# Performance work log

Hardware: AMD Instinct MI355X
Metric: run time of the kernel (lower is better)

## Reference

```python
import jax, jax.numpy as jnp
import numpy as np
from math import sqrt


def _build_transitions(dim):
    # Upper-triangular (i<=j) pairs in the same row-major order as the torch loop.
    iu0, iu1 = np.triu_indices(dim)
    n_mono = len(iu0)
    idx = np.arange(n_mono)
    M = np.zeros((dim, dim), dtype=np.int32)
    M[iu0, iu1] = idx
    M[iu1, iu0] = idx
    coef_trans = np.full((n_mono, 1), sqrt(2.0), dtype=np.float32)
    coef_trans[idx[iu0 == iu1]] = 1.0  # diagonal coefficients stay scale 1
    return iu0, iu1, M.reshape(-1), coef_trans


def setup_inputs() -> dict:
    key = jax.random.key(0)
    k1, k2, k3, k4 = jax.random.split(key, 4)
    dim, n_quadrics, B = 512, 64, 2048
    n_mono = dim * (dim - 1) // 2 + dim  # 131328
    points = jax.random.normal(k1, (B, dim), dtype=jnp.float32)
    # orthogonal-ish init is only an init detail; random normal keeps math identical
    q_coefs = jax.random.normal(k2, (n_mono, n_quadrics), dtype=jnp.float32) / np.sqrt(n_mono)
    l_coefs = 2.0 * jax.random.uniform(k3, (dim, n_quadrics), dtype=jnp.float32) - 1.0
    free_coefs = 2.0 * jax.random.uniform(k4, (1, n_quadrics), dtype=jnp.float32) - 1.0
    return {"points": points, "q_coefs": q_coefs, "l_coefs": l_coefs, "free_coefs": free_coefs}


def reference(points, q_coefs, l_coefs, free_coefs):
    B, dim = points.shape
    nq = q_coefs.shape[1]
    iu0, iu1, inds_trans, coef_trans_np = _build_transitions(dim)
    coef_trans = jnp.asarray(coef_trans_np)

    # quadratic monomials: q[b, k] = p[b, i_k] * p[b, j_k]  (upper-tri order)
    q = points[:, iu0] * points[:, iu1]  # (B, n_mono)

    coefs = q_coefs * coef_trans  # (n_mono, nq) real coefficients

    # values of quadrics at points
    values = jnp.abs(q @ coefs + points @ l_coefs + free_coefs)  # (B, nq)

    # symmetric full matrices gathered from flat coefficient vector
    m_full = coefs[inds_trans].reshape(dim, dim, nq)  # (dim, dim, nq)
    dm = (jnp.eye(dim, dtype=points.dtype) + 1.0)[:, :, None]  # 2 on diag, ... wait: eye+ones -> 2 diag, 1 off
    m_scaled = m_full * dm

    # gradients: grad[b, k, e] = sum_d p[b, d] * m_scaled[d, e, k] + l_coefs[e, k]
    q_grad = jnp.einsum("bd,dek->bke", points, m_scaled) + l_coefs.T[None, :, :]  # (B, nq, dim)
    grad = jnp.sum(q_grad * q_grad, axis=2)  # (B, nq)

    norm = jnp.linalg.norm(q_coefs, axis=0)  # (nq,)
    scores = (jnp.sqrt(grad / 4.0 + values * norm) - jnp.sqrt(grad) / 2.0) / norm
    return scores
```

## Files before the change

kernel.cpp:

```cpp
#include <hip/hip_runtime.h>

#define DIM 512
#define NQ 64
#define BATCH 2048

typedef __bf16  bf16x8  __attribute__((ext_vector_type(8)));
typedef float   floatx4 __attribute__((ext_vector_type(4)));

static __device__ inline unsigned short f2bf(float f) {
    unsigned int u = __float_as_uint(f);
    return (unsigned short)((u + 0x7fffu + ((u >> 16) & 1u)) >> 16);
}
static __device__ inline float bf2f(unsigned short h) {
    return __uint_as_float((unsigned int)h << 16);
}
static __device__ inline unsigned int pack2(float a, float b) {
    return (unsigned)f2bf(a) | ((unsigned)f2bf(b) << 16);
}

__global__ __launch_bounds__(512, 3)
void hsq_expand_kernel(const float* __restrict__ qc,
                       const float* __restrict__ pts,
                       unsigned short* __restrict__ W,
                       unsigned short* __restrict__ Pb,
                       float* __restrict__ npart) {
    const int e = blockIdx.x;

    if (blockIdx.y == 4) {
        const int i4 = e * 512 + threadIdx.x;
        const float4 v = *(const float4*)(pts + (size_t)i4 * 4);
        uint2 wv;
        wv.x = pack2(v.x, v.y); wv.y = pack2(v.z, v.w);
        *(uint2*)(Pb + (size_t)i4 * 4) = wv;
        return;
    }

    const int dblk = blockIdx.y;
    const int pb   = dblk * 512 + e;
    const int tid  = threadIdx.x;
    const int w    = tid >> 6;
    const int lane = tid & 63;
    const int g    = lane >> 4;
    const int u    = lane & 15;
    const int d0   = dblk * 128;

    __shared__ unsigned short tv[64 * 136];
    __shared__ float part2[8][64];

    float4 nacc4 = {0.f, 0.f, 0.f, 0.f};

#pragma unroll
    for (int p = 0; p < 4; ++p) {
        const int rloc = p * 32 + w * 4;
        const int d = d0 + rloc + g;
        const int i = d < e ? d : e;
        const int j = d < e ? e : d;
        const int idx = i * DIM - ((i * (i - 1)) >> 1) + (j - i);
        float4 f = *(const float4*)(qc + (size_t)idx * NQ + u * 4);

        if (d >= e) {
            nacc4.x += f.x * f.x; nacc4.y += f.y * f.y;
            nacc4.z += f.z * f.z; nacc4.w += f.w * f.w;
        }
        const float s = (d == e) ? 2.0f : 1.41421356237309515f;
        float4 v = {f.x * s, f.y * s, f.z * s, f.w * s};

        {
            float s0 = (g & 2) ? v.x : v.z;
            float s1 = (g & 2) ? v.y : v.w;
            const float r0 = __shfl_xor(s0, 32);
            const float r1 = __shfl_xor(s1, 32);
            if (g & 2) { v.x = r0; v.y = r1; } else { v.z = r0; v.w = r1; }
        }
        {
            float s0 = (g & 1) ? v.x : v.y;
            float s1 = (g & 1) ? v.z : v.w;
            const float r0 = __shfl_xor(s0, 16);
            const float r1 = __shfl_xor(s1, 16);
            if (g & 1) { v.x = r0; v.z = r1; } else { v.y = r0; v.w = r1; }
        }
        const int k = u * 4 + g;
        uint2 wv;
        wv.x = pack2(v.x, v.y);
        wv.y = pack2(v.z, v.w);
        *(uint2*)&tv[k * 136 + rloc] = wv;
    }

    nacc4.x += __shfl_xor(nacc4.x, 16); nacc4.y += __shfl_xor(nacc4.y, 16);
    nacc4.z += __shfl_xor(nacc4.z, 16); nacc4.w += __shfl_xor(nacc4.w, 16);
    nacc4.x += __shfl_xor(nacc4.x, 32); nacc4.y += __shfl_xor(nacc4.y, 32);
    nacc4.z += __shfl_xor(nacc4.z, 32); nacc4.w += __shfl_xor(nacc4.w, 32);
    if (g == 0) *(float4*)&part2[w][u * 4] = nacc4;
    __syncthreads();

#pragma unroll
    for (int r = 0; r < 2; ++r) {
        const int kk = r * 32 + (tid >> 4);
        const int uu = tid & 15;
        const uint4 ww = *(const uint4*)&tv[kk * 136 + uu * 8];
        *(uint4*)(W + ((size_t)(kk * DIM + e)) * DIM + dblk * 128 + uu * 8) = ww;
    }
    if (tid < 64) {
        npart[(size_t)tid * 2048 + pb] =
            part2[0][tid] + part2[1][tid] + part2[2][tid] + part2[3][tid] +
            part2[4][tid] + part2[5][tid] + part2[6][tid] + part2[7][tid];
    }
}

__global__ __launch_bounds__(512, 2)
void hsq_gemm_kernel(const unsigned short* __restrict__ Pb,
                     const unsigned short* __restrict__ W,
                     const float* __restrict__ l_coefs,
                     float2* __restrict__ part) {
    extern __shared__ unsigned short smem[];

    const int bid = blockIdx.x;
    const int wg  = (bid & 7) * 128 + (bid >> 3);
    const int k   = wg >> 4;
    const int rem = wg & 15;
    const int et  = rem >> 3;
    const int mt  = rem & 7;
    const int m0  = mt * 256;

    const int tid  = threadIdx.x;
    const int lane = tid & 63;
    const int w    = tid >> 6;
    const int wm   = w >> 2;
    const int wn   = w & 3;
    const int c    = lane & 15;
    const int quad = lane >> 4;

    const unsigned short* Wk = W + ((size_t)k * DIM + (size_t)et * 256) * DIM;

    const int scolb = ((tid & 7) * 16) ^ (((tid >> 3) & 7) << 4);
    const unsigned short* pAs = Pb + (size_t)(m0 + (tid >> 3)) * DIM + (scolb >> 1);
    const unsigned short* pBs = Wk + (size_t)(tid >> 3) * DIM + (scolb >> 1);

    const int xorv  = (c & 7) << 4;
    const int koff0 = ((0 * 64 + quad * 16) ^ xorv) >> 1;
    const int koff1 = ((1 * 64 + quad * 16) ^ xorv) >> 1;
    const int awoff = wm * 8192 + c * 64;
    const int bwoff = (wn >> 1) * 8192 + (wn & 1) * 4096 + c * 64;

#define STAGE_HALF(LDSELEM, GSRC) do {                                         \
    _Pragma("unroll")                                                          \
    for (int cc_ = 0; cc_ < 2; ++cc_) {                                        \
        __builtin_amdgcn_global_load_lds(                                      \
            (const __attribute__((address_space(1))) unsigned int*)            \
                ((GSRC) + (size_t)(cc_ * 64) * DIM),                           \
            (__attribute__((address_space(3))) unsigned int*)                  \
                (smem + (LDSELEM) + cc_ * 4096 + tid * 8),                     \
            16, 0, 0);                                                         \
    }                                                                          \
} while (0)

#define LOADB(BBASE) do {                                                      \
    _Pragma("unroll")                                                          \
    for (int ni_ = 0; ni_ < 4; ++ni_) {                                        \
        bfr[ni_][0] = *(const bf16x8*)(smem + (BBASE) + bwoff + ni_ * 1024 + koff0); \
        bfr[ni_][1] = *(const bf16x8*)(smem + (BBASE) + bwoff + ni_ * 1024 + koff1); \
    }                                                                          \
} while (0)

#define PHASE(ABASE, MI0, PRE_B, STAGE_AND_WAIT) do {                          \
    bf16x8 a00 = *(const bf16x8*)(smem + (ABASE) + awoff + (MI0) * 1024 + koff0);     \
    bf16x8 a01 = *(const bf16x8*)(smem + (ABASE) + awoff + (MI0) * 1024 + koff1);     \
    bf16x8 a10 = *(const bf16x8*)(smem + (ABASE) + awoff + ((MI0) + 1) * 1024 + koff0); \
    bf16x8 a11 = *(const bf16x8*)(smem + (ABASE) + awoff + ((MI0) + 1) * 1024 + koff1); \
    PRE_B;                                                                     \
    STAGE_AND_WAIT;                                                            \
    asm volatile("" ::: "memory");                                             \
    __builtin_amdgcn_s_barrier();                                              \
    asm volatile("" ::: "memory");                                             \
    __builtin_amdgcn_s_setprio(1);                                             \
    _Pragma("unroll")                                                          \
    for (int ni_ = 0; ni_ < 4; ++ni_) {                                        \
        acc[(MI0)][ni_]     = __builtin_amdgcn_mfma_f32_16x16x32_bf16(a00, bfr[ni_][0], acc[(MI0)][ni_], 0, 0, 0);     \
        acc[(MI0)][ni_]     = __builtin_amdgcn_mfma_f32_16x16x32_bf16(a01, bfr[ni_][1], acc[(MI0)][ni_], 0, 0, 0);     \
        acc[(MI0) + 1][ni_] = __builtin_amdgcn_mfma_f32_16x16x32_bf16(a10, bfr[ni_][0], acc[(MI0) + 1][ni_], 0, 0, 0); \
        acc[(MI0) + 1][ni_] = __builtin_amdgcn_mfma_f32_16x16x32_bf16(a11, bfr[ni_][1], acc[(MI0) + 1][ni_], 0, 0, 0); \
    }                                                                          \
    __builtin_amdgcn_s_setprio(0);                                             \
    asm volatile("" ::: "memory");                                             \
    __builtin_amdgcn_s_barrier();                                              \
    asm volatile("" ::: "memory");                                             \
} while (0)

    floatx4 acc[8][4];
#pragma unroll
    for (int mi = 0; mi < 8; ++mi)
#pragma unroll
        for (int ni = 0; ni < 4; ++ni)
            acc[mi][ni] = (floatx4){0.f, 0.f, 0.f, 0.f};

    bf16x8 bfr[4][2];

    STAGE_HALF(0,             pAs);
    STAGE_HALF(8192,          pAs + 128 * DIM);
    STAGE_HALF(16384,         pBs);
    STAGE_HALF(16384 + 8192,  pBs + 128 * DIM);
    STAGE_HALF(49152,         pBs + 64);
    STAGE_HALF(49152 + 8192,  pBs + 128 * DIM + 64);
    asm volatile("s_waitcnt vmcnt(4)" ::: "memory");
    __builtin_amdgcn_s_barrier();
    asm volatile("" ::: "memory");

    for (int it = 0; it < 4; ++it) {
        const unsigned short* pA1 = pAs + (size_t)(2 * it + 1) * 64;
        const unsigned short* pB2 = pBs + (size_t)(2 * it + 2) * 64;
        const unsigned short* pA2 = pAs + (size_t)(2 * it + 2) * 64;
        const unsigned short* pB3 = pBs + (size_t)(2 * it + 3) * 64;

        PHASE(0, 0, LOADB(16384), { STAGE_HALF(32768, pA1); });
        PHASE(0, 2, ((void)0),    { STAGE_HALF(32768 + 8192, pA1 + 128 * DIM); });
        PHASE(0, 4, ((void)0),    { if (it < 3) STAGE_HALF(16384, pB2); });
        PHASE(0, 6, ((void)0), {
            if (it < 3) {
                STAGE_HALF(16384 + 8192, pB2 + 128 * DIM);
                asm volatile("s_waitcnt vmcnt(4)" ::: "memory");
            } else {
                asm volatile("s_waitcnt vmcnt(0)" ::: "memory");
            }
        });
        PHASE(32768, 0, LOADB(49152), { if (it < 3) STAGE_HALF(0, pA2); });
        PHASE(32768, 2, ((void)0),    { if (it < 3) STAGE_HALF(8192, pA2 + 128 * DIM); });
        PHASE(32768, 4, ((void)0),    { if (it < 3) STAGE_HALF(49152, pB3); });
        PHASE(32768, 6, ((void)0), {
            if (it < 3) {
                STAGE_HALF(49152 + 8192, pB3 + 128 * DIM);
                asm volatile("s_waitcnt vmcnt(4)" ::: "memory");
            }
        });
    }
#undef PHASE
#undef LOADB
#undef STAGE_HALF

    __syncthreads();

    float lcv[4];
#pragma unroll
    for (int ni = 0; ni < 4; ++ni)
        lcv[ni] = l_coefs[(et * 256 + wn * 64 + ni * 16 + c) * NQ + k];

    const unsigned short* Pe = Pb + (size_t)(m0 + wm * 128) * DIM + et * 256 + wn * 64 + c;
    float* red = (float*)smem;

#pragma unroll
    for (int mi = 0; mi < 8; ++mi)
#pragma unroll
        for (int r = 0; r < 4; ++r) {
            const unsigned short* Prow = Pe + (size_t)(mi * 16 + quad * 4 + r) * DIM;
            float pv = 0.f, pg = 0.f;
#pragma unroll
            for (int ni = 0; ni < 4; ++ni) {
                const float g = acc[mi][ni][r];
                const float l = lcv[ni];
                pv += bf2f(Prow[ni * 16]) * (0.5f * g + l);
                const float gq = g + l;
                pg += gq * gq;
            }
#pragma unroll
            for (int off = 1; off < 16; off <<= 1) {
                pv += __shfl_xor(pv, off);
                pg += __shfl_xor(pg, off);
            }
            if (c == 0) {
                const int row16 = mi * 16 + quad * 4 + r;
                red[(w * 128 + row16) * 2 + 0] = pv;
                red[(w * 128 + row16) * 2 + 1] = pg;
            }
        }
    __syncthreads();

    if (tid < 256) {
        const int row16 = tid & 127;
        const int wmf   = tid >> 7;
        float pv = 0.f, pg = 0.f;
#pragma unroll
        for (int wnf = 0; wnf < 4; ++wnf) {
            const int wi = wmf * 4 + wnf;
            pv += red[(wi * 128 + row16) * 2 + 0];
            pg += red[(wi * 128 + row16) * 2 + 1];
        }
        part[((size_t)(et * NQ + k)) * BATCH + m0 + wmf * 128 + row16] =
            make_float2(pv, pg);
    }
}

__global__ void hsq_final_kernel(const float2* __restrict__ part,
                                 const float* __restrict__ npart,
                                 const float* __restrict__ free_coefs,
                                 float* __restrict__ out) {
    const int k = blockIdx.x;
    const int t = threadIdx.x;
    __shared__ float ws[4];

    const float4* src = (const float4*)(npart + (size_t)k * 2048);
    const float4 a = src[t * 2], b = src[t * 2 + 1];
    float s = a.x + a.y + a.z + a.w + b.x + b.y + b.z + b.w;
#pragma unroll
    for (int off = 1; off < 64; off <<= 1) s += __shfl_xor(s, off);
    if ((t & 63) == 0) ws[t >> 6] = s;
    __syncthreads();
    const float nrm = sqrtf(ws[0] + ws[1] + ws[2] + ws[3]);
    const float fc  = free_coefs[k];

#pragma unroll
    for (int i = 0; i < 8; ++i) {
        const int bidx = i * 256 + t;
        float pv = 0.f, pg = 0.f;
#pragma unroll
        for (int eb = 0; eb < 2; ++eb) {
            const float2 p = part[((size_t)(eb * NQ + k)) * BATCH + bidx];
            pv += p.x; pg += p.y;
        }
        const float vals = fabsf(pv + fc);
        out[(size_t)bidx * NQ + k] = (sqrtf(0.25f * pg + vals * nrm) - 0.5f * sqrtf(pg)) / nrm;
    }
}

extern "C" void kernel_launch(void* const* d_in, const int* in_sizes, int n_in,
                              void* d_out, int out_size, void* d_ws, size_t ws_size,
                              hipStream_t stream) {
    const float* points     = (const float*)d_in[0];
    const float* q_coefs    = (const float*)d_in[1];
    const float* l_coefs    = (const float*)d_in[2];
    const float* free_coefs = (const float*)d_in[3];
    float* out = (float*)d_out;

    char* ws = (char*)d_ws;
    unsigned short* W  = (unsigned short*)ws;
    unsigned short* Pb = (unsigned short*)(ws + 33554432);
    float2*         part  = (float2*)(ws + 35651584);
    float*          npart = (float*)(ws + 37748736);

    static bool attr_done = false;
    if (!attr_done) {
        (void)hipFuncSetAttribute((const void*)hsq_gemm_kernel,
                                  hipFuncAttributeMaxDynamicSharedMemorySize,
                                  131072);
        attr_done = true;
    }

    hsq_expand_kernel<<<dim3(512, 5), 512, 0, stream>>>(q_coefs, points, W, Pb, npart);
    hsq_gemm_kernel<<<dim3(1024), dim3(512), 131072, stream>>>(Pb, W, l_coefs, part);
    hsq_final_kernel<<<dim3(NQ), 256, 0, stream>>>(part, npart, free_coefs, out);
}
```

Measured before the change: 190.5 us.

## Split GEMM tile across 16 waves with double-buffered 64-wide k stages

The GEMM kernel now launches 1024 threads instead of 512, so each wave owns a 64x64 output sub-tile (4x4 MFMA accumulators) instead of 128x64. The LDS staging becomes a simpler two-buffer A/B scheme with 64-wide k chunks and fewer, larger async copies per phase. The epilogue reduction is remapped to the new wave layout. This aims for more waves to hide latency and less register pressure per wave. In exchange there is more barrier traffic per MFMA, and the aggressive launch bounds may force register spills.

Result: slower. 231.4 us (+21.4%).

```diff
diff --git a/kernel.cpp b/kernel.cpp
--- a/kernel.cpp
+++ b/kernel.cpp
@@ -107,7 +107,7 @@
     }
 }
 
-__global__ __launch_bounds__(512, 2)
+__global__ __launch_bounds__(1024, 4)
 void hsq_gemm_kernel(const unsigned short* __restrict__ Pb,
                      const unsigned short* __restrict__ W,
                      const float* __restrict__ l_coefs,
@@ -136,37 +136,40 @@
     const unsigned short* pAs = Pb + (size_t)(m0 + (tid >> 3)) * DIM + (scolb >> 1);
     const unsigned short* pBs = Wk + (size_t)(tid >> 3) * DIM + (scolb >> 1);
 
-    const int xorv  = (c & 7) << 4;
-    const int koff0 = ((0 * 64 + quad * 16) ^ xorv) >> 1;
-    const int koff1 = ((1 * 64 + quad * 16) ^ xorv) >> 1;
-    const int awoff = wm * 8192 + c * 64;
-    const int bwoff = (wn >> 1) * 8192 + (wn & 1) * 4096 + c * 64;
-
-#define STAGE_HALF(LDSELEM, GSRC) do {                                         \
+    const int koff0 = ((0 * 64 + quad * 16) ^ ((c & 7) << 4)) >> 1;
+    const int koff1 = ((1 * 64 + quad * 16) ^ ((c & 7) << 4)) >> 1;
+    const int awoff = wm * 4096 + c * 64;
+    const int bwoff = wn * 4096 + c * 64;
+
+#define AELEM(BUF) ((BUF) * 32768)
+#define BELEM(BUF) ((BUF) * 32768 + 16384)
+
+#define STAGE2(DSTELEM, GSRC) do {                                             \
+    __builtin_amdgcn_global_load_lds(                                          \
+        (const __attribute__((address_space(1))) unsigned int*)(GSRC),         \
+        (__attribute__((address_space(3))) unsigned int*)                      \
+            (smem + (DSTELEM) + tid * 8), 16, 0, 0);                           \
+    __builtin_amdgcn_global_load_lds(                                          \
+        (const __attribute__((address_space(1))) unsigned int*)                \
+            ((GSRC) + 128 * DIM),                                              \
+        (__attribute__((address_space(3))) unsigned int*)                      \
+            (smem + (DSTELEM) + 8192 + tid * 8), 16, 0, 0);                    \
+} while (0)
+
+#define LOADB(BUF) do {                                                        \
     _Pragma("unroll")                                                          \
-    for (int cc_ = 0; cc_ < 2; ++cc_) {                                        \
-        __builtin_amdgcn_global_load_lds(                                      \
-            (const __attribute__((address_space(1))) unsigned int*)            \
-                ((GSRC) + (size_t)(cc_ * 64) * DIM),                           \
-            (__attribute__((address_space(3))) unsigned int*)                  \
-                (smem + (LDSELEM) + cc_ * 4096 + tid * 8),                     \
-            16, 0, 0);                                                         \
+    for (int ni_ = 0; ni_ < 4; ++ni_) {                                        \
+        bfr[ni_][0] = *(const bf16x8*)(smem + BELEM(BUF) + bwoff + ni_ * 1024 + koff0); \
+        bfr[ni_][1] = *(const bf16x8*)(smem + BELEM(BUF) + bwoff + ni_ * 1024 + koff1); \
     }                                                                          \
 } while (0)
 
-#define LOADB(BBASE) do {                                                      \
+#define PHASE(BUF, KH, PRE_B, STAGE_AND_WAIT) do {                             \
+    bf16x8 afr[4];                                                             \
     _Pragma("unroll")                                                          \
-    for (int ni_ = 0; ni_ < 4; ++ni_) {                                        \
-        bfr[ni_][0] = *(const bf16x8*)(smem + (BBASE) + bwoff + ni_ * 1024 + koff0); \
-        bfr[ni_][1] = *(const bf16x8*)(smem + (BBASE) + bwoff + ni_ * 1024 + koff1); \
-    }                                                                          \
-} while (0)
-
-#define PHASE(ABASE, MI0, PRE_B, STAGE_AND_WAIT) do {                          \
-    bf16x8 a00 = *(const bf16x8*)(smem + (ABASE) + awoff + (MI0) * 1024 + koff0);     \
-    bf16x8 a01 = *(const bf16x8*)(smem + (ABASE) + awoff + (MI0) * 1024 + koff1);     \
-    bf16x8 a10 = *(const bf16x8*)(smem + (ABASE) + awoff + ((MI0) + 1) * 1024 + koff0); \
-    bf16x8 a11 = *(const bf16x8*)(smem + (ABASE) + awoff + ((MI0) + 1) * 1024 + koff1); \
+    for (int mi_ = 0; mi_ < 4; ++mi_)                                          \
+        afr[mi_] = *(const bf16x8*)(smem + AELEM(BUF) + awoff + mi_ * 1024 +   \
+                                    ((KH) ? koff1 : koff0));                   \
     PRE_B;                                                                     \
     STAGE_AND_WAIT;                                                            \
     asm volatile("" ::: "memory");                                             \
@@ -174,67 +177,59 @@
     asm volatile("" ::: "memory");                                             \
     __builtin_amdgcn_s_setprio(1);                                             \
     _Pragma("unroll")                                                          \
-    for (int ni_ = 0; ni_ < 4; ++ni_) {                                        \
-        acc[(MI0)][ni_]     = __builtin_amdgcn_mfma_f32_16x16x32_bf16(a00, bfr[ni_][0], acc[(MI0)][ni_], 0, 0, 0);     \
-        acc[(MI0)][ni_]     = __builtin_amdgcn_mfma_f32_16x16x32_bf16(a01, bfr[ni_][1], acc[(MI0)][ni_], 0, 0, 0);     \
-        acc[(MI0) + 1][ni_] = __builtin_amdgcn_mfma_f32_16x16x32_bf16(a10, bfr[ni_][0], acc[(MI0) + 1][ni_], 0, 0, 0); \
-        acc[(MI0) + 1][ni_] = __builtin_amdgcn_mfma_f32_16x16x32_bf16(a11, bfr[ni_][1], acc[(MI0) + 1][ni_], 0, 0, 0); \
-    }                                                                          \
+    for (int mi_ = 0; mi_ < 4; ++mi_)                                          \
+        _Pragma("unroll")                                                      \
+        for (int ni_ = 0; ni_ < 4; ++ni_)                                      \
+            acc[mi_][ni_] = __builtin_amdgcn_mfma_f32_16x16x32_bf16(           \
+                afr[mi_], bfr[ni_][KH], acc[mi_][ni_], 0, 0, 0);               \
     __builtin_amdgcn_s_setprio(0);                                             \
     asm volatile("" ::: "memory");                                             \
     __builtin_amdgcn_s_barrier();                                              \
     asm volatile("" ::: "memory");                                             \
 } while (0)
 
-    floatx4 acc[8][4];
-#pragma unroll
-    for (int mi = 0; mi < 8; ++mi)
+#define VM2  asm volatile("s_waitcnt vmcnt(2)" ::: "memory")
+#define VM0  asm volatile("s_waitcnt vmcnt(0)" ::: "memory")
+
+    floatx4 acc[4][4];
+#pragma unroll
+    for (int mi = 0; mi < 4; ++mi)
 #pragma unroll
         for (int ni = 0; ni < 4; ++ni)
             acc[mi][ni] = (floatx4){0.f, 0.f, 0.f, 0.f};
 
     bf16x8 bfr[4][2];
 
-    STAGE_HALF(0,             pAs);
-    STAGE_HALF(8192,          pAs + 128 * DIM);
-    STAGE_HALF(16384,         pBs);
-    STAGE_HALF(16384 + 8192,  pBs + 128 * DIM);
-    STAGE_HALF(49152,         pBs + 64);
-    STAGE_HALF(49152 + 8192,  pBs + 128 * DIM + 64);
-    asm volatile("s_waitcnt vmcnt(4)" ::: "memory");
+    STAGE2(AELEM(0), pAs);
+    STAGE2(BELEM(0), pBs);
+    STAGE2(BELEM(1), pBs + 64);
+    VM2;
     __builtin_amdgcn_s_barrier();
     asm volatile("" ::: "memory");
 
+#pragma unroll 1
     for (int it = 0; it < 4; ++it) {
         const unsigned short* pA1 = pAs + (size_t)(2 * it + 1) * 64;
+        const unsigned short* pA2 = pAs + (size_t)(2 * it + 2) * 64;
         const unsigned short* pB2 = pBs + (size_t)(2 * it + 2) * 64;
-        const unsigned short* pA2 = pAs + (size_t)(2 * it + 2) * 64;
         const unsigned short* pB3 = pBs + (size_t)(2 * it + 3) * 64;
 
-        PHASE(0, 0, LOADB(16384), { STAGE_HALF(32768, pA1); });
-        PHASE(0, 2, ((void)0),    { STAGE_HALF(32768 + 8192, pA1 + 128 * DIM); });
-        PHASE(0, 4, ((void)0),    { if (it < 3) STAGE_HALF(16384, pB2); });
-        PHASE(0, 6, ((void)0), {
-            if (it < 3) {
-                STAGE_HALF(16384 + 8192, pB2 + 128 * DIM);
-                asm volatile("s_waitcnt vmcnt(4)" ::: "memory");
-            } else {
-                asm volatile("s_waitcnt vmcnt(0)" ::: "memory");
-            }
+        PHASE(0, 0, LOADB(0), { STAGE2(AELEM(1), pA1); });
+        PHASE(0, 1, ((void)0), {
+            if (it < 3) { STAGE2(BELEM(0), pB2); VM2; } else { VM0; }
         });
-        PHASE(32768, 0, LOADB(49152), { if (it < 3) STAGE_HALF(0, pA2); });
-        PHASE(32768, 2, ((void)0),    { if (it < 3) STAGE_HALF(8192, pA2 + 128 * DIM); });
-        PHASE(32768, 4, ((void)0),    { if (it < 3) STAGE_HALF(49152, pB3); });
-        PHASE(32768, 6, ((void)0), {
-            if (it < 3) {
-                STAGE_HALF(49152 + 8192, pB3 + 128 * DIM);
-                asm volatile("s_waitcnt vmcnt(4)" ::: "memory");
-            }
+        PHASE(1, 0, LOADB(1), { if (it < 3) STAGE2(AELEM(0), pA2); });
+        PHASE(1, 1, ((void)0), {
+            if (it < 3) { STAGE2(BELEM(1), pB3); VM2; }
         });
     }
 #undef PHASE
 #undef LOADB
-#undef STAGE_HALF
+#undef STAGE2
+#undef AELEM
+#undef BELEM
+#undef VM2
+#undef VM0
 
     __syncthreads();
 
@@ -243,11 +238,11 @@
     for (int ni = 0; ni < 4; ++ni)
         lcv[ni] = l_coefs[(et * 256 + wn * 64 + ni * 16 + c) * NQ + k];
 
-    const unsigned short* Pe = Pb + (size_t)(m0 + wm * 128) * DIM + et * 256 + wn * 64 + c;
+    const unsigned short* Pe = Pb + (size_t)(m0 + wm * 64) * DIM + et * 256 + wn * 64 + c;
     float* red = (float*)smem;
 
 #pragma unroll
-    for (int mi = 0; mi < 8; ++mi)
+    for (int mi = 0; mi < 4; ++mi)
 #pragma unroll
         for (int r = 0; r < 4; ++r) {
             const unsigned short* Prow = Pe + (size_t)(mi * 16 + quad * 4 + r) * DIM;
@@ -266,25 +261,21 @@
                 pg += __shfl_xor(pg, off);
             }
             if (c == 0) {
-                const int row16 = mi * 16 + quad * 4 + r;
-                red[(w * 128 + row16) * 2 + 0] = pv;
-                red[(w * 128 + row16) * 2 + 1] = pg;
+                const int row = wm * 64 + mi * 16 + quad * 4 + r;
+                red[(wn * 256 + row) * 2 + 0] = pv;
+                red[(wn * 256 + row) * 2 + 1] = pg;
             }
         }
     __syncthreads();
 
     if (tid < 256) {
-        const int row16 = tid & 127;
-        const int wmf   = tid >> 7;
         float pv = 0.f, pg = 0.f;
 #pragma unroll
         for (int wnf = 0; wnf < 4; ++wnf) {
-            const int wi = wmf * 4 + wnf;
-            pv += red[(wi * 128 + row16) * 2 + 0];
-            pg += red[(wi * 128 + row16) * 2 + 1];
-        }
-        part[((size_t)(et * NQ + k)) * BATCH + m0 + wmf * 128 + row16] =
-            make_float2(pv, pg);
+            pv += red[(wnf * 256 + tid) * 2 + 0];
+            pg += red[(wnf * 256 + tid) * 2 + 1];
+        }
+        part[((size_t)(et * NQ + k)) * BATCH + m0 + tid] = make_float2(pv, pg);
     }
 }
 
@@ -344,6 +335,6 @@
     }
 
     hsq_expand_kernel<<<dim3(512, 5), 512, 0, stream>>>(q_coefs, points, W, Pb, npart);
-    hsq_gemm_kernel<<<dim3(1024), dim3(512), 131072, stream>>>(Pb, W, l_coefs, part);
+    hsq_gemm_kernel<<<dim3(1024), dim3(1024), 131072, stream>>>(Pb, W, l_coefs, part);
     hsq_final_kernel<<<dim3(NQ), 256, 0, stream>>>(part, npart, free_coefs, out);
 }
```

## Load A fragments directly from global, stage only B in LDS

Applied to the files above, without the earlier changes.

The GEMM main loop no longer stages the points (A) tile through LDS. Each wave loads its A fragments straight from global memory into registers, and only the W (B) tile is double-buffered in LDS, so LDS use drops from 128KB to 64KB. The change cuts LDS traffic and may allow two workgroups per CU. The cost is uncoalesced, latency-exposed global loads of A inside the loop, plus a full vmcnt(0) wait and barrier every K-tile, which reduces overlap.

After: 271.8 us. +42.6%, slower.

```diff
diff --git a/kernel.cpp b/kernel.cpp
--- a/kernel.cpp
+++ b/kernel.cpp
@@ -133,55 +133,61 @@
     const unsigned short* Wk = W + ((size_t)k * DIM + (size_t)et * 256) * DIM;
 
     const int scolb = ((tid & 7) * 16) ^ (((tid >> 3) & 7) << 4);
-    const unsigned short* pAs = Pb + (size_t)(m0 + (tid >> 3)) * DIM + (scolb >> 1);
     const unsigned short* pBs = Wk + (size_t)(tid >> 3) * DIM + (scolb >> 1);
 
-    const int xorv  = (c & 7) << 4;
-    const int koff0 = ((0 * 64 + quad * 16) ^ xorv) >> 1;
-    const int koff1 = ((1 * 64 + quad * 16) ^ xorv) >> 1;
-    const int awoff = wm * 8192 + c * 64;
-    const int bwoff = (wn >> 1) * 8192 + (wn & 1) * 4096 + c * 64;
-
-#define STAGE_HALF(LDSELEM, GSRC) do {                                         \
-    _Pragma("unroll")                                                          \
-    for (int cc_ = 0; cc_ < 2; ++cc_) {                                        \
+    const unsigned short* pA = Pb + (size_t)(m0 + wm * 128 + c) * DIM + quad * 8;
+
+    const int koff0 = ((0 * 64 + quad * 16) ^ ((c & 7) << 4)) >> 1;
+    const int koff1 = ((1 * 64 + quad * 16) ^ ((c & 7) << 4)) >> 1;
+    const int bwoff = (wn * 64 + c) * 64;
+
+#define STAGE_B(BUF, T) do {                                                   \
+    const unsigned short* src_ = pBs + (size_t)(T) * 64;                       \
+    _Pragma("unroll")                                                          \
+    for (int cc_ = 0; cc_ < 4; ++cc_) {                                        \
         __builtin_amdgcn_global_load_lds(                                      \
             (const __attribute__((address_space(1))) unsigned int*)            \
-                ((GSRC) + (size_t)(cc_ * 64) * DIM),                           \
+                (src_ + (size_t)(cc_ * 64) * DIM),                             \
             (__attribute__((address_space(3))) unsigned int*)                  \
-                (smem + (LDSELEM) + cc_ * 4096 + tid * 8),                     \
+                (smem + (BUF) * 16384 + cc_ * 4096 + tid * 8),                 \
             16, 0, 0);                                                         \
     }                                                                          \
 } while (0)
 
-#define LOADB(BBASE) do {                                                      \
+#define KTILE(BUF, T, DO_STAGE) do {                                           \
+    bf16x8 bfr[4][2];                                                          \
     _Pragma("unroll")                                                          \
     for (int ni_ = 0; ni_ < 4; ++ni_) {                                        \
-        bfr[ni_][0] = *(const bf16x8*)(smem + (BBASE) + bwoff + ni_ * 1024 + koff0); \
-        bfr[ni_][1] = *(const bf16x8*)(smem + (BBASE) + bwoff + ni_ * 1024 + koff1); \
+        bfr[ni_][0] = *(const bf16x8*)(smem + (BUF) * 16384 + bwoff + ni_ * 1024 + koff0); \
+        bfr[ni_][1] = *(const bf16x8*)(smem + (BUF) * 16384 + bwoff + ni_ * 1024 + koff1); \
     }                                                                          \
-} while (0)
-
-#define PHASE(ABASE, MI0, PRE_B, STAGE_AND_WAIT) do {                          \
-    bf16x8 a00 = *(const bf16x8*)(smem + (ABASE) + awoff + (MI0) * 1024 + koff0);     \
-    bf16x8 a01 = *(const bf16x8*)(smem + (ABASE) + awoff + (MI0) * 1024 + koff1);     \
-    bf16x8 a10 = *(const bf16x8*)(smem + (ABASE) + awoff + ((MI0) + 1) * 1024 + koff0); \
-    bf16x8 a11 = *(const bf16x8*)(smem + (ABASE) + awoff + ((MI0) + 1) * 1024 + koff1); \
-    PRE_B;                                                                     \
-    STAGE_AND_WAIT;                                                            \
+    bf16x8 afr[8];                                                             \
+    _Pragma("unroll")                                                          \
+    for (int mi_ = 0; mi_ < 8; ++mi_)                                          \
+        afr[mi_] = *(const bf16x8*)(pA + (size_t)mi_ * 16 * DIM + (T) * 64);   \
     asm volatile("" ::: "memory");                                             \
-    __builtin_amdgcn_s_barrier();                                              \
+    DO_STAGE;                                                                  \
     asm volatile("" ::: "memory");                                             \
     __builtin_amdgcn_s_setprio(1);                                             \
     _Pragma("unroll")                                                          \
-    for (int ni_ = 0; ni_ < 4; ++ni_) {                                        \
-        acc[(MI0)][ni_]     = __builtin_amdgcn_mfma_f32_16x16x32_bf16(a00, bfr[ni_][0], acc[(MI0)][ni_], 0, 0, 0);     \
-        acc[(MI0)][ni_]     = __builtin_amdgcn_mfma_f32_16x16x32_bf16(a01, bfr[ni_][1], acc[(MI0)][ni_], 0, 0, 0);     \
-        acc[(MI0) + 1][ni_] = __builtin_amdgcn_mfma_f32_16x16x32_bf16(a10, bfr[ni_][0], acc[(MI0) + 1][ni_], 0, 0, 0); \
-        acc[(MI0) + 1][ni_] = __builtin_amdgcn_mfma_f32_16x16x32_bf16(a11, bfr[ni_][1], acc[(MI0) + 1][ni_], 0, 0, 0); \
-    }                                                                          \
+    for (int mi_ = 0; mi_ < 8; ++mi_)                                          \
+        _Pragma("unroll")                                                      \
+        for (int ni_ = 0; ni_ < 4; ++ni_)                                      \
+            acc[mi_][ni_] = __builtin_amdgcn_mfma_f32_16x16x32_bf16(           \
+                afr[mi_], bfr[ni_][0], acc[mi_][ni_], 0, 0, 0);                \
     __builtin_amdgcn_s_setprio(0);                                             \
-    asm volatile("" ::: "memory");                                             \
+    _Pragma("unroll")                                                          \
+    for (int mi_ = 0; mi_ < 8; ++mi_)                                          \
+        afr[mi_] = *(const bf16x8*)(pA + (size_t)mi_ * 16 * DIM + (T) * 64 + 32); \
+    __builtin_amdgcn_s_setprio(1);                                             \
+    _Pragma("unroll")                                                          \
+    for (int mi_ = 0; mi_ < 8; ++mi_)                                          \
+        _Pragma("unroll")                                                      \
+        for (int ni_ = 0; ni_ < 4; ++ni_)                                      \
+            acc[mi_][ni_] = __builtin_amdgcn_mfma_f32_16x16x32_bf16(           \
+                afr[mi_], bfr[ni_][1], acc[mi_][ni_], 0, 0, 0);                \
+    __builtin_amdgcn_s_setprio(0);                                             \
+    asm volatile("s_waitcnt vmcnt(0)" ::: "memory");                           \
     __builtin_amdgcn_s_barrier();                                              \
     asm volatile("" ::: "memory");                                             \
 } while (0)
@@ -193,48 +199,18 @@
         for (int ni = 0; ni < 4; ++ni)
             acc[mi][ni] = (floatx4){0.f, 0.f, 0.f, 0.f};
 
-    bf16x8 bfr[4][2];
-
-    STAGE_HALF(0,             pAs);
-    STAGE_HALF(8192,          pAs + 128 * DIM);
-    STAGE_HALF(16384,         pBs);
-    STAGE_HALF(16384 + 8192,  pBs + 128 * DIM);
-    STAGE_HALF(49152,         pBs + 64);
-    STAGE_HALF(49152 + 8192,  pBs + 128 * DIM + 64);
-    asm volatile("s_waitcnt vmcnt(4)" ::: "memory");
+    STAGE_B(0, 0);
+    asm volatile("s_waitcnt vmcnt(0)" ::: "memory");
     __builtin_amdgcn_s_barrier();
     asm volatile("" ::: "memory");
 
+#pragma unroll 1
     for (int it = 0; it < 4; ++it) {
-        const unsigned short* pA1 = pAs + (size_t)(2 * it + 1) * 64;
-        const unsigned short* pB2 = pBs + (size_t)(2 * it + 2) * 64;
-        const unsigned short* pA2 = pAs + (size_t)(2 * it + 2) * 64;
-        const unsigned short* pB3 = pBs + (size_t)(2 * it + 3) * 64;
-
-        PHASE(0, 0, LOADB(16384), { STAGE_HALF(32768, pA1); });
-        PHASE(0, 2, ((void)0),    { STAGE_HALF(32768 + 8192, pA1 + 128 * DIM); });
-        PHASE(0, 4, ((void)0),    { if (it < 3) STAGE_HALF(16384, pB2); });
-        PHASE(0, 6, ((void)0), {
-            if (it < 3) {
-                STAGE_HALF(16384 + 8192, pB2 + 128 * DIM);
-                asm volatile("s_waitcnt vmcnt(4)" ::: "memory");
-            } else {
-                asm volatile("s_waitcnt vmcnt(0)" ::: "memory");
-            }
-        });
-        PHASE(32768, 0, LOADB(49152), { if (it < 3) STAGE_HALF(0, pA2); });
-        PHASE(32768, 2, ((void)0),    { if (it < 3) STAGE_HALF(8192, pA2 + 128 * DIM); });
-        PHASE(32768, 4, ((void)0),    { if (it < 3) STAGE_HALF(49152, pB3); });
-        PHASE(32768, 6, ((void)0), {
-            if (it < 3) {
-                STAGE_HALF(49152 + 8192, pB3 + 128 * DIM);
-                asm volatile("s_waitcnt vmcnt(4)" ::: "memory");
-            }
-        });
-    }
-#undef PHASE
-#undef LOADB
-#undef STAGE_HALF
+        KTILE(0, 2 * it,     { if (true)   STAGE_B(1, 2 * it + 1); });
+        KTILE(1, 2 * it + 1, { if (it < 3) STAGE_B(0, 2 * it + 2); });
+    }
+#undef KTILE
+#undef STAGE_B
 
     __syncthreads();
 
@@ -339,11 +315,11 @@
     if (!attr_done) {
         (void)hipFuncSetAttribute((const void*)hsq_gemm_kernel,
                                   hipFuncAttributeMaxDynamicSharedMemorySize,
-                                  131072);
+                                  65536);
         attr_done = true;
     }
 
     hsq_expand_kernel<<<dim3(512, 5), 512, 0, stream>>>(q_coefs, points, W, Pb, npart);
-    hsq_gemm_kernel<<<dim3(1024), dim3(512), 131072, stream>>>(Pb, W, l_coefs, part);
+    hsq_gemm_kernel<<<dim3(1024), dim3(512), 65536, stream>>>(Pb, W, l_coefs, part);
     hsq_final_kernel<<<dim3(NQ), 256, 0, stream>>>(part, npart, free_coefs, out);
 }
```

## Process two quadrics per GEMM workgroup with continuous prefetch across boundary

Applied to the files above, without the earlier changes.

Each GEMM workgroup now handles two consecutive quadrics (k0, k0+1), so the grid shrinks from 1024 to 512 blocks. The A/B staging pipeline carries on across the quadric boundary: the first epilogue runs while the loads for the second quadric are already in flight. A separate LDS reduction region is added so the epilogue does not clash with staging buffers, which raises LDS to 139264 bytes. This trims the pipeline prologue/drain cost per quadric, but LDS use grows and there are fewer workgroups to spread across CUs.

Result: slower. 234.0 us (+22.8%).

```diff
diff --git a/kernel.cpp b/kernel.cpp
--- a/kernel.cpp
+++ b/kernel.cpp
@@ -114,13 +114,14 @@
                      float2* __restrict__ part) {
     extern __shared__ unsigned short smem[];
 
-    const int bid = blockIdx.x;
-    const int wg  = (bid & 7) * 128 + (bid >> 3);
-    const int k   = wg >> 4;
-    const int rem = wg & 15;
-    const int et  = rem >> 3;
-    const int mt  = rem & 7;
-    const int m0  = mt * 256;
+    const int bid   = blockIdx.x;
+    const int wg    = (bid & 7) * 64 + (bid >> 3);
+    const int kpair = wg >> 4;
+    const int rem   = wg & 15;
+    const int et    = rem >> 3;
+    const int mt    = rem & 7;
+    const int m0    = mt * 256;
+    const int k0    = kpair * 2;
 
     const int tid  = threadIdx.x;
     const int lane = tid & 63;
@@ -130,17 +131,22 @@
     const int c    = lane & 15;
     const int quad = lane >> 4;
 
-    const unsigned short* Wk = W + ((size_t)k * DIM + (size_t)et * 256) * DIM;
+    const unsigned short* Wk = W + ((size_t)k0 * DIM + (size_t)et * 256) * DIM;
 
     const int scolb = ((tid & 7) * 16) ^ (((tid >> 3) & 7) << 4);
     const unsigned short* pAs = Pb + (size_t)(m0 + (tid >> 3)) * DIM + (scolb >> 1);
     const unsigned short* pBs = Wk + (size_t)(tid >> 3) * DIM + (scolb >> 1);
+#define PA(g) (pAs + (size_t)((g) & 7) * 64)
+#define PB(g) (pBs + (size_t)((g) >> 3) * (DIM * DIM) + (size_t)((g) & 7) * 64)
 
     const int xorv  = (c & 7) << 4;
     const int koff0 = ((0 * 64 + quad * 16) ^ xorv) >> 1;
     const int koff1 = ((1 * 64 + quad * 16) ^ xorv) >> 1;
     const int awoff = wm * 8192 + c * 64;
     const int bwoff = (wn >> 1) * 8192 + (wn & 1) * 4096 + c * 64;
+
+    const unsigned short* Pe = Pb + (size_t)(m0 + wm * 128) * DIM + et * 256 + wn * 64 + c;
+    float* red = (float*)&smem[65536];
 
 #define STAGE_HALF(LDSELEM, GSRC) do {                                         \
     _Pragma("unroll")                                                          \
@@ -186,6 +192,54 @@
     asm volatile("" ::: "memory");                                             \
 } while (0)
 
+#define EPILOG(KK) do {                                                        \
+    float lcv[4];                                                              \
+    _Pragma("unroll")                                                          \
+    for (int ni = 0; ni < 4; ++ni)                                             \
+        lcv[ni] = l_coefs[(et * 256 + wn * 64 + ni * 16 + c) * NQ + (KK)];     \
+    _Pragma("unroll")                                                          \
+    for (int mi = 0; mi < 8; ++mi)                                             \
+        _Pragma("unroll")                                                      \
+        for (int r = 0; r < 4; ++r) {                                          \
+            const unsigned short* Prow = Pe + (size_t)(mi * 16 + quad * 4 + r) * DIM; \
+            float pv = 0.f, pg = 0.f;                                          \
+            _Pragma("unroll")                                                  \
+            for (int ni = 0; ni < 4; ++ni) {                                   \
+                const float g = acc[mi][ni][r];                                \
+                const float l = lcv[ni];                                       \
+                pv += bf2f(Prow[ni * 16]) * (0.5f * g + l);                    \
+                const float gq = g + l;                                        \
+                pg += gq * gq;                                                 \
+            }                                                                  \
+            _Pragma("unroll")                                                  \
+            for (int off = 1; off < 16; off <<= 1) {                           \
+                pv += __shfl_xor(pv, off);                                     \
+                pg += __shfl_xor(pg, off);                                     \
+            }                                                                  \
+            if (c == 0) {                                                      \
+                const int row16 = mi * 16 + quad * 4 + r;                      \
+                red[(w * 128 + row16) * 2 + 0] = pv;                           \
+                red[(w * 128 + row16) * 2 + 1] = pg;                           \
+            }                                                                  \
+        }                                                                      \
+    asm volatile("s_waitcnt lgkmcnt(0)" ::: "memory");                         \
+    __builtin_amdgcn_s_barrier();                                              \
+    asm volatile("" ::: "memory");                                             \
+    if (tid < 256) {                                                           \
+        const int row16 = tid & 127;                                           \
+        const int wmf   = tid >> 7;                                            \
+        float pv = 0.f, pg = 0.f;                                              \
+        _Pragma("unroll")                                                      \
+        for (int wnf = 0; wnf < 4; ++wnf) {                                    \
+            const int wi = wmf * 4 + wnf;                                      \
+            pv += red[(wi * 128 + row16) * 2 + 0];                             \
+            pg += red[(wi * 128 + row16) * 2 + 1];                             \
+        }                                                                      \
+        part[((size_t)(et * NQ + (KK))) * BATCH + m0 + wmf * 128 + row16] =    \
+            make_float2(pv, pg);                                               \
+    }                                                                          \
+} while (0)
+
     floatx4 acc[8][4];
 #pragma unroll
     for (int mi = 0; mi < 8; ++mi)
@@ -195,97 +249,71 @@
 
     bf16x8 bfr[4][2];
 
-    STAGE_HALF(0,             pAs);
-    STAGE_HALF(8192,          pAs + 128 * DIM);
-    STAGE_HALF(16384,         pBs);
-    STAGE_HALF(16384 + 8192,  pBs + 128 * DIM);
-    STAGE_HALF(49152,         pBs + 64);
-    STAGE_HALF(49152 + 8192,  pBs + 128 * DIM + 64);
+    STAGE_HALF(0,             PA(0));
+    STAGE_HALF(8192,          PA(0) + 128 * DIM);
+    STAGE_HALF(16384,         PB(0));
+    STAGE_HALF(16384 + 8192,  PB(0) + 128 * DIM);
+    STAGE_HALF(49152,         PB(1));
+    STAGE_HALF(49152 + 8192,  PB(1) + 128 * DIM);
     asm volatile("s_waitcnt vmcnt(4)" ::: "memory");
     __builtin_amdgcn_s_barrier();
     asm volatile("" ::: "memory");
 
+#pragma unroll 1
     for (int it = 0; it < 4; ++it) {
-        const unsigned short* pA1 = pAs + (size_t)(2 * it + 1) * 64;
-        const unsigned short* pB2 = pBs + (size_t)(2 * it + 2) * 64;
-        const unsigned short* pA2 = pAs + (size_t)(2 * it + 2) * 64;
-        const unsigned short* pB3 = pBs + (size_t)(2 * it + 3) * 64;
-
-        PHASE(0, 0, LOADB(16384), { STAGE_HALF(32768, pA1); });
-        PHASE(0, 2, ((void)0),    { STAGE_HALF(32768 + 8192, pA1 + 128 * DIM); });
-        PHASE(0, 4, ((void)0),    { if (it < 3) STAGE_HALF(16384, pB2); });
+        const int g1 = 2 * it + 1, g2 = 2 * it + 2, g3 = 2 * it + 3;
+        PHASE(0, 0, LOADB(16384), { STAGE_HALF(32768, PA(g1)); });
+        PHASE(0, 2, ((void)0),    { STAGE_HALF(32768 + 8192, PA(g1) + 128 * DIM); });
+        PHASE(0, 4, ((void)0),    { STAGE_HALF(16384, PB(g2)); });
+        PHASE(0, 6, ((void)0),    { STAGE_HALF(16384 + 8192, PB(g2) + 128 * DIM);
+                                    asm volatile("s_waitcnt vmcnt(4)" ::: "memory"); });
+        PHASE(32768, 0, LOADB(49152), { STAGE_HALF(0, PA(g2)); });
+        PHASE(32768, 2, ((void)0),    { STAGE_HALF(8192, PA(g2) + 128 * DIM); });
+        PHASE(32768, 4, ((void)0),    { STAGE_HALF(49152, PB(g3)); });
+        PHASE(32768, 6, ((void)0),    { STAGE_HALF(49152 + 8192, PB(g3) + 128 * DIM);
+                                        asm volatile("s_waitcnt vmcnt(4)" ::: "memory"); });
+    }
+
+    EPILOG(k0);
+#pragma unroll
+    for (int mi = 0; mi < 8; ++mi)
+#pragma unroll
+        for (int ni = 0; ni < 4; ++ni)
+            acc[mi][ni] = (floatx4){0.f, 0.f, 0.f, 0.f};
+
+#pragma unroll 1
+    for (int it = 4; it < 8; ++it) {
+        const int g1 = 2 * it + 1, g2 = 2 * it + 2, g3 = 2 * it + 3;
+        PHASE(0, 0, LOADB(16384), { STAGE_HALF(32768, PA(g1)); });
+        PHASE(0, 2, ((void)0),    { STAGE_HALF(32768 + 8192, PA(g1) + 128 * DIM); });
+        PHASE(0, 4, ((void)0),    { if (it < 7) STAGE_HALF(16384, PB(g2)); });
         PHASE(0, 6, ((void)0), {
-            if (it < 3) {
-                STAGE_HALF(16384 + 8192, pB2 + 128 * DIM);
+            if (it < 7) {
+                STAGE_HALF(16384 + 8192, PB(g2) + 128 * DIM);
                 asm volatile("s_waitcnt vmcnt(4)" ::: "memory");
             } else {
                 asm volatile("s_waitcnt vmcnt(0)" ::: "memory");
             }
         });
-        PHASE(32768, 0, LOADB(49152), { if (it < 3) STAGE_HALF(0, pA2); });
-        PHASE(32768, 2, ((void)0),    { if (it < 3) STAGE_HALF(8192, pA2 + 128 * DIM); });
-        PHASE(32768, 4, ((void)0),    { if (it < 3) STAGE_HALF(49152, pB3); });
+        PHASE(32768, 0, LOADB(49152), { if (it < 7) STAGE_HALF(0, PA(g2)); });
+        PHASE(32768, 2, ((void)0),    { if (it < 7) STAGE_HALF(8192, PA(g2) + 128 * DIM); });
+        PHASE(32768, 4, ((void)0),    { if (it < 7) STAGE_HALF(49152, PB(g3)); });
         PHASE(32768, 6, ((void)0), {
-            if (it < 3) {
-                STAGE_HALF(49152 + 8192, pB3 + 128 * DIM);
+            if (it < 7) {
+                STAGE_HALF(49152 + 8192, PB(g3) + 128 * DIM);
                 asm volatile("s_waitcnt vmcnt(4)" ::: "memory");
             }
         });
     }
+
+    EPILOG(k0 + 1);
+
 #undef PHASE
 #undef LOADB
 #undef STAGE_HALF
-
-    __syncthreads();
-
-    float lcv[4];
-#pragma unroll
-    for (int ni = 0; ni < 4; ++ni)
-        lcv[ni] = l_coefs[(et * 256 + wn * 64 + ni * 16 + c) * NQ + k];
-
-    const unsigned short* Pe = Pb + (size_t)(m0 + wm * 128) * DIM + et * 256 + wn * 64 + c;
-    float* red = (float*)smem;
-
-#pragma unroll
-    for (int mi = 0; mi < 8; ++mi)
-#pragma unroll
-        for (int r = 0; r < 4; ++r) {
-            const unsigned short* Prow = Pe + (size_t)(mi * 16 + quad * 4 + r) * DIM;
-            float pv = 0.f, pg = 0.f;
-#pragma unroll
-            for (int ni = 0; ni < 4; ++ni) {
-                const float g = acc[mi][ni][r];
-                const float l = lcv[ni];
-                pv += bf2f(Prow[ni * 16]) * (0.5f * g + l);
-                const float gq = g + l;
-                pg += gq * gq;
-            }
-#pragma unroll
-            for (int off = 1; off < 16; off <<= 1) {
-                pv += __shfl_xor(pv, off);
-                pg += __shfl_xor(pg, off);
-            }
-            if (c == 0) {
-                const int row16 = mi * 16 + quad * 4 + r;
-                red[(w * 128 + row16) * 2 + 0] = pv;
-                red[(w * 128 + row16) * 2 + 1] = pg;
-            }
-        }
-    __syncthreads();
-
-    if (tid < 256) {
-        const int row16 = tid & 127;
-        const int wmf   = tid >> 7;
-        float pv = 0.f, pg = 0.f;
-#pragma unroll
-        for (int wnf = 0; wnf < 4; ++wnf) {
-            const int wi = wmf * 4 + wnf;
-            pv += red[(wi * 128 + row16) * 2 + 0];
-            pg += red[(wi * 128 + row16) * 2 + 1];
-        }
-        part[((size_t)(et * NQ + k)) * BATCH + m0 + wmf * 128 + row16] =
-            make_float2(pv, pg);
-    }
+#undef EPILOG
+#undef PA
+#undef PB
 }
 
 __global__ void hsq_final_kernel(const float2* __restrict__ part,
@@ -339,11 +367,11 @@
     if (!attr_done) {
         (void)hipFuncSetAttribute((const void*)hsq_gemm_kernel,
                                   hipFuncAttributeMaxDynamicSharedMemorySize,
-                                  131072);
+                                  139264);
         attr_done = true;
     }
 
     hsq_expand_kernel<<<dim3(512, 5), 512, 0, stream>>>(q_coefs, points, W, Pb, npart);
-    hsq_gemm_kernel<<<dim3(1024), dim3(512), 131072, stream>>>(Pb, W, l_coefs, part);
+    hsq_gemm_kernel<<<dim3(512), dim3(512), 139264, stream>>>(Pb, W, l_coefs, part);
     hsq_final_kernel<<<dim3(NQ), 256, 0, stream>>>(part, npart, free_coefs, out);
 }
```
